# Kernel optimization log

Hardware: AMD Instinct MI355X
Metric: run time of the kernel (lower is better)

The kernel has to match this reference:

```python
import jax, jax.numpy as jnp
import numpy as np


def setup_inputs() -> dict:
    key = jax.random.key(0)
    ks = jax.random.split(key, 5)
    b, t, q_dim, kv_dim, h = 16, 128, 256, 64, 4
    c = t - 1
    q_x = jax.random.normal(ks[0], (b, t, q_dim), dtype=jnp.float32)
    kv_x = jax.random.normal(ks[1], (b, t, c, kv_dim), dtype=jnp.float32)
    # Linear weights stored as [in, out]; no biases (bias=False in torch module).
    sq = 1.0 / np.sqrt(q_dim)
    sk = 1.0 / np.sqrt(kv_dim)
    Wq = jax.random.uniform(ks[2], (q_dim, kv_dim * h), jnp.float32, -sq, sq)
    Wk = jax.random.uniform(ks[3], (kv_dim, kv_dim * h), jnp.float32, -sk, sk)
    Wv = jax.random.uniform(ks[4], (kv_dim, kv_dim * h), jnp.float32, -sk, sk)
    return {"q_x": q_x, "kv_x": kv_x, "Wq": Wq, "Wk": Wk, "Wv": Wv}


def reference(q_x, kv_x, Wq, Wk, Wv):
    b, t, c, k = kv_x.shape  # c = t - 1
    h = Wq.shape[1] // k
    # projections
    q = (q_x @ Wq).reshape(b, t, h, k)          # [b,t,h,k]
    keys = (kv_x @ Wk).reshape(b, t, c, h, k)   # [b,t,c,h,k]
    vals = (kv_x @ Wv).reshape(b, t, c, h, k)
    # per-token attention over the c-sized context
    scores = jnp.einsum('bthk,btchk->bthc', q, keys) / jnp.sqrt(jnp.float32(k))
    w = jax.nn.softmax(scores, axis=-1)          # softmax over context dim
    out = jnp.einsum('bthc,btchk->bthk', w, vals)
    return out.reshape(b, t, h * k)
```

## Files before the change

kernel.cpp:

```cpp
#include <hip/hip_runtime.h>
#include <math.h>

#define Bdim 16
#define Tdim 128
#define Cdim 127
#define Hdim 4
#define QD   256
#define HK   256
#define BT   (Bdim * Tdim)

#define DPP_XOR1        0xB1
#define DPP_XOR2        0x4E
#define DPP_HALF_MIRROR 0x141
#define DPP_MIRROR      0x140
template<int CTRL>
__device__ __forceinline__ float dpp_movf(float x) {
    return __int_as_float(__builtin_amdgcn_update_dpp(
        0, __float_as_int(x), CTRL, 0xF, 0xF, true));
}

__global__ __launch_bounds__(256) void qk_fused(
        const float* __restrict__ q_x,
        const float* __restrict__ Wq,
        const float* __restrict__ Wk,
        float* __restrict__ qk) {
    __shared__ __align__(16) float q_s[4][256];
    __shared__ __align__(16) float p_s[4][4][68];
    int RB = blockIdx.x;
    int tid = threadIdx.x;
    {
        int r = tid >> 6, kq = tid & 63;
        *(float4*)&q_s[r][kq*4] =
            *(const float4*)(q_x + (size_t)(RB*4 + r) * QD + kq * 4);
    }
    __syncthreads();

    float acc[4] = {0.f, 0.f, 0.f, 0.f};
    #pragma unroll 4
    for (int i4 = 0; i4 < 64; ++i4) {
        float w0 = Wq[(size_t)(4*i4+0) * HK + tid];
        float w1 = Wq[(size_t)(4*i4+1) * HK + tid];
        float w2 = Wq[(size_t)(4*i4+2) * HK + tid];
        float w3 = Wq[(size_t)(4*i4+3) * HK + tid];
        #pragma unroll
        for (int r = 0; r < 4; ++r) {
            float4 qv = *(const float4*)&q_s[r][i4*4];
            acc[r] = fmaf(qv.x, w0, fmaf(qv.y, w1, fmaf(qv.z, w2, fmaf(qv.w, w3, acc[r]))));
        }
    }
    int h = tid >> 6, m = tid & 63;
    #pragma unroll
    for (int r = 0; r < 4; ++r) p_s[r][h][m] = acc[r];
    __syncthreads();

    const float4* wk4 = (const float4*)(Wk + (size_t)m * HK + h * 64);
    float4 wkr[16];
    #pragma unroll
    for (int j = 0; j < 16; ++j) wkr[j] = wk4[j];
    float a2[4] = {0.f, 0.f, 0.f, 0.f};
    #pragma unroll
    for (int j4 = 0; j4 < 16; ++j4) {
        #pragma unroll
        for (int r = 0; r < 4; ++r) {
            float4 pv = *(const float4*)&p_s[r][h][j4*4];
            a2[r] = fmaf(pv.x, wkr[j4].x, fmaf(pv.y, wkr[j4].y,
                    fmaf(pv.z, wkr[j4].z, fmaf(pv.w, wkr[j4].w, a2[r]))));
        }
    }
    #pragma unroll
    for (int r = 0; r < 4; ++r)
        qk[(size_t)(RB*4 + r) * HK + tid] = a2[r];
}

__global__ __launch_bounds__(256, 6) void attn_main(
        const float* __restrict__ kv_x,
        const float* __restrict__ qk_g,
        const float* __restrict__ Wv,
        float* __restrict__ out) {
    __shared__ __align__(16) float qk_s[HK];
    __shared__ __align__(16) float4 e4[128];
    __shared__ __align__(16) float4 wx4[Hdim * 16];
    __shared__ __align__(16) float4 reds[4];

    int bt  = blockIdx.x;
    int tid = threadIdx.x;
    const float* Xr = kv_x + (size_t)bt * (Cdim * 64);

    qk_s[tid] = qk_g[(size_t)bt * HK + tid];
    __syncthreads();

    int lane = tid & 63;
    int wave = tid >> 6;

    float e0, e1, e2, e3;
    {
        int c  = tid >> 1;
        int hf = tid & 1;
        bool valid = (c < Cdim);
        int crow = valid ? c : 0;
        const float4* xq = (const float4*)(Xr + crow * 64) + hf * 8;
        const float4* qk4 = (const float4*)qk_s;
        float a0 = 0.f, a1 = 0.f, a2 = 0.f, a3 = 0.f;
        #pragma unroll
        for (int i = 0; i < 8; ++i) {
            float4 xi = xq[i];
            float4 q0 = qk4[0*16 + hf*8 + i];
            float4 q1 = qk4[1*16 + hf*8 + i];
            float4 q2 = qk4[2*16 + hf*8 + i];
            float4 q3 = qk4[3*16 + hf*8 + i];
            a0 = fmaf(q0.x, xi.x, fmaf(q0.y, xi.y, fmaf(q0.z, xi.z, fmaf(q0.w, xi.w, a0))));
            a1 = fmaf(q1.x, xi.x, fmaf(q1.y, xi.y, fmaf(q1.z, xi.z, fmaf(q1.w, xi.w, a1))));
            a2 = fmaf(q2.x, xi.x, fmaf(q2.y, xi.y, fmaf(q2.z, xi.z, fmaf(q2.w, xi.w, a2))));
            a3 = fmaf(q3.x, xi.x, fmaf(q3.y, xi.y, fmaf(q3.z, xi.z, fmaf(q3.w, xi.w, a3))));
        }
        a0 += dpp_movf<DPP_XOR1>(a0);
        a1 += dpp_movf<DPP_XOR1>(a1);
        a2 += dpp_movf<DPP_XOR1>(a2);
        a3 += dpp_movf<DPP_XOR1>(a3);
        e0 = valid ? __expf(a0 * 0.125f) : 0.f;
        e1 = valid ? __expf(a1 * 0.125f) : 0.f;
        e2 = valid ? __expf(a2 * 0.125f) : 0.f;
        e3 = valid ? __expf(a3 * 0.125f) : 0.f;
        if (hf == 0) e4[c] = make_float4(e0, e1, e2, e3);
    }
    float t0 = e0, t1 = e1, t2 = e2, t3 = e3;
    t0 += dpp_movf<DPP_XOR2>(t0); t1 += dpp_movf<DPP_XOR2>(t1);
    t2 += dpp_movf<DPP_XOR2>(t2); t3 += dpp_movf<DPP_XOR2>(t3);
    t0 += dpp_movf<DPP_HALF_MIRROR>(t0); t1 += dpp_movf<DPP_HALF_MIRROR>(t1);
    t2 += dpp_movf<DPP_HALF_MIRROR>(t2); t3 += dpp_movf<DPP_HALF_MIRROR>(t3);
    t0 += dpp_movf<DPP_MIRROR>(t0); t1 += dpp_movf<DPP_MIRROR>(t1);
    t2 += dpp_movf<DPP_MIRROR>(t2); t3 += dpp_movf<DPP_MIRROR>(t3);
    t0 += __shfl_xor(t0, 16, 64); t1 += __shfl_xor(t1, 16, 64);
    t2 += __shfl_xor(t2, 16, 64); t3 += __shfl_xor(t3, 16, 64);
    t0 += __shfl_xor(t0, 32, 64); t1 += __shfl_xor(t1, 32, 64);
    t2 += __shfl_xor(t2, 32, 64); t3 += __shfl_xor(t3, 32, 64);
    if (lane == 0) reds[wave] = make_float4(t0, t1, t2, t3);
    __syncthreads();

    {
        int jc = tid >> 4;
        int g  = tid & 15;
        float4 A0 = {0,0,0,0}, A1 = {0,0,0,0}, A2 = {0,0,0,0}, A3 = {0,0,0,0};
        #pragma unroll
        for (int mm = 0; mm < 8; ++mm) {
            int cc = g + 16 * mm;
            int ccrow = (cc < Cdim) ? cc : 0;
            float4 x4 = *(const float4*)(Xr + ccrow * 64 + jc * 4);
            float4 ee = e4[cc];
            A0.x = fmaf(ee.x, x4.x, A0.x); A0.y = fmaf(ee.x, x4.y, A0.y);
            A0.z = fmaf(ee.x, x4.z, A0.z); A0.w = fmaf(ee.x, x4.w, A0.w);
            A1.x = fmaf(ee.y, x4.x, A1.x); A1.y = fmaf(ee.y, x4.y, A1.y);
            A1.z = fmaf(ee.y, x4.z, A1.z); A1.w = fmaf(ee.y, x4.w, A1.w);
            A2.x = fmaf(ee.z, x4.x, A2.x); A2.y = fmaf(ee.z, x4.y, A2.y);
            A2.z = fmaf(ee.z, x4.z, A2.z); A2.w = fmaf(ee.z, x4.w, A2.w);
            A3.x = fmaf(ee.w, x4.x, A3.x); A3.y = fmaf(ee.w, x4.y, A3.y);
            A3.z = fmaf(ee.w, x4.z, A3.z); A3.w = fmaf(ee.w, x4.w, A3.w);
        }
        #define WXRED(v) \
            v += dpp_movf<DPP_XOR1>(v); \
            v += dpp_movf<DPP_XOR2>(v); \
            v += dpp_movf<DPP_HALF_MIRROR>(v); \
            v += dpp_movf<DPP_MIRROR>(v);
        WXRED(A0.x) WXRED(A0.y) WXRED(A0.z) WXRED(A0.w)
        WXRED(A1.x) WXRED(A1.y) WXRED(A1.z) WXRED(A1.w)
        WXRED(A2.x) WXRED(A2.y) WXRED(A2.z) WXRED(A2.w)
        WXRED(A3.x) WXRED(A3.y) WXRED(A3.z) WXRED(A3.w)
        #undef WXRED
        if ((lane & 15) == 0) {
            wx4[0 * 16 + jc] = A0;
            wx4[1 * 16 + jc] = A1;
            wx4[2 * 16 + jc] = A2;
            wx4[3 * 16 + jc] = A3;
        }
    }
    __syncthreads();

    {
        int hh = tid >> 6, k = tid & 63;
        float4 s0 = reds[0], s1 = reds[1], s2 = reds[2], s3 = reds[3];
        float4 sums = make_float4(s0.x+s1.x+s2.x+s3.x, s0.y+s1.y+s2.y+s3.y,
                                  s0.z+s1.z+s2.z+s3.z, s0.w+s1.w+s2.w+s3.w);
        float denom = (hh == 0) ? sums.x : (hh == 1) ? sums.y
                    : (hh == 2) ? sums.z : sums.w;
        float inv = 1.f / denom;
        const float* wvcol = Wv + hh * 64 + k;
        float acc = 0.f;
        #pragma unroll 4
        for (int jc = 0; jc < 16; ++jc) {
            float4 w4 = wx4[hh * 16 + jc];
            acc = fmaf(w4.x, wvcol[(size_t)(jc*4+0) * HK],
                  fmaf(w4.y, wvcol[(size_t)(jc*4+1) * HK],
                  fmaf(w4.z, wvcol[(size_t)(jc*4+2) * HK],
                  fmaf(w4.w, wvcol[(size_t)(jc*4+3) * HK], acc))));
        }
        out[(size_t)bt * HK + tid] = acc * inv;
    }
}

extern "C" void kernel_launch(void* const* d_in, const int* in_sizes, int n_in,
                              void* d_out, int out_size, void* d_ws, size_t ws_size,
                              hipStream_t stream) {
    const float* q_x  = (const float*)d_in[0];
    const float* kv_x = (const float*)d_in[1];
    const float* Wq   = (const float*)d_in[2];
    const float* Wk   = (const float*)d_in[3];
    const float* Wv   = (const float*)d_in[4];
    float* out = (float*)d_out;

    float* qk = (float*)d_ws;

    qk_fused<<<BT / 4, 256, 0, stream>>>(q_x, Wq, Wk, qk);
    attn_main<<<BT, 256, 0, stream>>>(kv_x, qk, Wv, out);
}
```

Before: 42.55 us.

## Stage kv_x rows in swizzled LDS and prefetch next token while computing

Each attn_main block now handles two (b,t) tokens. It stages the 127x64 kv_x tile into XOR-swizzled shared memory, and loads the second token's tile into registers while the first token is computed, so global latency overlaps compute. Both the score pass and the weighted-sum pass read kv_x from LDS instead of issuing two separate global reads. The cost is about 32KB of LDS, a lower occupancy hint, half as many blocks (1024), and 32 extra registers for the prefetch.

```diff
diff --git a/kernel.cpp b/kernel.cpp
--- a/kernel.cpp
+++ b/kernel.cpp
@@ -72,128 +72,170 @@
         qk[(size_t)(RB*4 + r) * HK + tid] = a2[r];
 }
 
-__global__ __launch_bounds__(256, 6) void attn_main(
+__global__ __launch_bounds__(256, 4) void attn_main(
         const float* __restrict__ kv_x,
         const float* __restrict__ qk_g,
         const float* __restrict__ Wv,
         float* __restrict__ out) {
+    __shared__ __align__(16) float4 sX4[128 * 16];
     __shared__ __align__(16) float qk_s[HK];
     __shared__ __align__(16) float4 e4[128];
     __shared__ __align__(16) float4 wx4[Hdim * 16];
     __shared__ __align__(16) float4 reds[4];
 
-    int bt  = blockIdx.x;
     int tid = threadIdx.x;
-    const float* Xr = kv_x + (size_t)bt * (Cdim * 64);
-
-    qk_s[tid] = qk_g[(size_t)bt * HK + tid];
-    __syncthreads();
-
     int lane = tid & 63;
     int wave = tid >> 6;
-
-    float e0, e1, e2, e3;
+    int bt0 = blockIdx.x * 2;
+
+    int src_off[8];
+    #pragma unroll
+    for (int k = 0; k < 8; ++k) {
+        int l = tid + 256 * k;
+        int c = l >> 4, p = l & 15;
+        src_off[k] = (l < Cdim * 16) ? ((c << 4) + (p ^ (c & 7))) : 0;
+    }
+
+    float4 P[8];
+    float qkp;
     {
+        const float4* Xg = (const float4*)(kv_x + (size_t)bt0 * (Cdim * 64));
+        #pragma unroll
+        for (int k = 0; k < 8; ++k) P[k] = Xg[src_off[k]];
+        qkp = qk_g[(size_t)bt0 * HK + tid];
+    }
+    #pragma unroll
+    for (int k = 0; k < 8; ++k) {
+        int l = tid + 256 * k;
+        sX4[l] = (l < Cdim * 16) ? P[k] : make_float4(0.f, 0.f, 0.f, 0.f);
+    }
+    qk_s[tid] = qkp;
+    __syncthreads();
+
+    #pragma unroll
+    for (int it = 0; it < 2; ++it) {
+        int bt = bt0 + it;
+
+        if (it == 0) {
+            const float4* Xg = (const float4*)(kv_x + (size_t)(bt0+1) * (Cdim * 64));
+            #pragma unroll
+            for (int k = 0; k < 8; ++k) P[k] = Xg[src_off[k]];
+            qkp = qk_g[(size_t)(bt0+1) * HK + tid];
+        }
+
+        float e0, e1, e2, e3;
         int c  = tid >> 1;
-        int hf = tid & 1;
-        bool valid = (c < Cdim);
-        int crow = valid ? c : 0;
-        const float4* xq = (const float4*)(Xr + crow * 64) + hf * 8;
-        const float4* qk4 = (const float4*)qk_s;
-        float a0 = 0.f, a1 = 0.f, a2 = 0.f, a3 = 0.f;
-        #pragma unroll
-        for (int i = 0; i < 8; ++i) {
-            float4 xi = xq[i];
-            float4 q0 = qk4[0*16 + hf*8 + i];
-            float4 q1 = qk4[1*16 + hf*8 + i];
-            float4 q2 = qk4[2*16 + hf*8 + i];
-            float4 q3 = qk4[3*16 + hf*8 + i];
-            a0 = fmaf(q0.x, xi.x, fmaf(q0.y, xi.y, fmaf(q0.z, xi.z, fmaf(q0.w, xi.w, a0))));
-            a1 = fmaf(q1.x, xi.x, fmaf(q1.y, xi.y, fmaf(q1.z, xi.z, fmaf(q1.w, xi.w, a1))));
-            a2 = fmaf(q2.x, xi.x, fmaf(q2.y, xi.y, fmaf(q2.z, xi.z, fmaf(q2.w, xi.w, a2))));
-            a3 = fmaf(q3.x, xi.x, fmaf(q3.y, xi.y, fmaf(q3.z, xi.z, fmaf(q3.w, xi.w, a3))));
-        }
-        a0 += dpp_movf<DPP_XOR1>(a0);
-        a1 += dpp_movf<DPP_XOR1>(a1);
-        a2 += dpp_movf<DPP_XOR1>(a2);
-        a3 += dpp_movf<DPP_XOR1>(a3);
-        e0 = valid ? __expf(a0 * 0.125f) : 0.f;
-        e1 = valid ? __expf(a1 * 0.125f) : 0.f;
-        e2 = valid ? __expf(a2 * 0.125f) : 0.f;
-        e3 = valid ? __expf(a3 * 0.125f) : 0.f;
-        if (hf == 0) e4[c] = make_float4(e0, e1, e2, e3);
-    }
-    float t0 = e0, t1 = e1, t2 = e2, t3 = e3;
-    t0 += dpp_movf<DPP_XOR2>(t0); t1 += dpp_movf<DPP_XOR2>(t1);
-    t2 += dpp_movf<DPP_XOR2>(t2); t3 += dpp_movf<DPP_XOR2>(t3);
-    t0 += dpp_movf<DPP_HALF_MIRROR>(t0); t1 += dpp_movf<DPP_HALF_MIRROR>(t1);
-    t2 += dpp_movf<DPP_HALF_MIRROR>(t2); t3 += dpp_movf<DPP_HALF_MIRROR>(t3);
-    t0 += dpp_movf<DPP_MIRROR>(t0); t1 += dpp_movf<DPP_MIRROR>(t1);
-    t2 += dpp_movf<DPP_MIRROR>(t2); t3 += dpp_movf<DPP_MIRROR>(t3);
-    t0 += __shfl_xor(t0, 16, 64); t1 += __shfl_xor(t1, 16, 64);
-    t2 += __shfl_xor(t2, 16, 64); t3 += __shfl_xor(t3, 16, 64);
-    t0 += __shfl_xor(t0, 32, 64); t1 += __shfl_xor(t1, 32, 64);
-    t2 += __shfl_xor(t2, 32, 64); t3 += __shfl_xor(t3, 32, 64);
-    if (lane == 0) reds[wave] = make_float4(t0, t1, t2, t3);
-    __syncthreads();
-
-    {
-        int jc = tid >> 4;
-        int g  = tid & 15;
-        float4 A0 = {0,0,0,0}, A1 = {0,0,0,0}, A2 = {0,0,0,0}, A3 = {0,0,0,0};
-        #pragma unroll
-        for (int mm = 0; mm < 8; ++mm) {
-            int cc = g + 16 * mm;
-            int ccrow = (cc < Cdim) ? cc : 0;
-            float4 x4 = *(const float4*)(Xr + ccrow * 64 + jc * 4);
-            float4 ee = e4[cc];
-            A0.x = fmaf(ee.x, x4.x, A0.x); A0.y = fmaf(ee.x, x4.y, A0.y);
-            A0.z = fmaf(ee.x, x4.z, A0.z); A0.w = fmaf(ee.x, x4.w, A0.w);
-            A1.x = fmaf(ee.y, x4.x, A1.x); A1.y = fmaf(ee.y, x4.y, A1.y);
-            A1.z = fmaf(ee.y, x4.z, A1.z); A1.w = fmaf(ee.y, x4.w, A1.w);
-            A2.x = fmaf(ee.z, x4.x, A2.x); A2.y = fmaf(ee.z, x4.y, A2.y);
-            A2.z = fmaf(ee.z, x4.z, A2.z); A2.w = fmaf(ee.z, x4.w, A2.w);
-            A3.x = fmaf(ee.w, x4.x, A3.x); A3.y = fmaf(ee.w, x4.y, A3.y);
-            A3.z = fmaf(ee.w, x4.z, A3.z); A3.w = fmaf(ee.w, x4.w, A3.w);
-        }
-        #define WXRED(v) \
-            v += dpp_movf<DPP_XOR1>(v); \
-            v += dpp_movf<DPP_XOR2>(v); \
-            v += dpp_movf<DPP_HALF_MIRROR>(v); \
-            v += dpp_movf<DPP_MIRROR>(v);
-        WXRED(A0.x) WXRED(A0.y) WXRED(A0.z) WXRED(A0.w)
-        WXRED(A1.x) WXRED(A1.y) WXRED(A1.z) WXRED(A1.w)
-        WXRED(A2.x) WXRED(A2.y) WXRED(A2.z) WXRED(A2.w)
-        WXRED(A3.x) WXRED(A3.y) WXRED(A3.z) WXRED(A3.w)
-        #undef WXRED
-        if ((lane & 15) == 0) {
-            wx4[0 * 16 + jc] = A0;
-            wx4[1 * 16 + jc] = A1;
-            wx4[2 * 16 + jc] = A2;
-            wx4[3 * 16 + jc] = A3;
-        }
-    }
-    __syncthreads();
-
-    {
-        int hh = tid >> 6, k = tid & 63;
-        float4 s0 = reds[0], s1 = reds[1], s2 = reds[2], s3 = reds[3];
-        float4 sums = make_float4(s0.x+s1.x+s2.x+s3.x, s0.y+s1.y+s2.y+s3.y,
-                                  s0.z+s1.z+s2.z+s3.z, s0.w+s1.w+s2.w+s3.w);
-        float denom = (hh == 0) ? sums.x : (hh == 1) ? sums.y
-                    : (hh == 2) ? sums.z : sums.w;
-        float inv = 1.f / denom;
-        const float* wvcol = Wv + hh * 64 + k;
-        float acc = 0.f;
-        #pragma unroll 4
-        for (int jc = 0; jc < 16; ++jc) {
-            float4 w4 = wx4[hh * 16 + jc];
-            acc = fmaf(w4.x, wvcol[(size_t)(jc*4+0) * HK],
-                  fmaf(w4.y, wvcol[(size_t)(jc*4+1) * HK],
-                  fmaf(w4.z, wvcol[(size_t)(jc*4+2) * HK],
-                  fmaf(w4.w, wvcol[(size_t)(jc*4+3) * HK], acc))));
-        }
-        out[(size_t)bt * HK + tid] = acc * inv;
+        {
+            int hf = tid & 1;
+            int sw = c & 7;
+            bool valid = (c < Cdim);
+            const float4* xrow = sX4 + c * 16;
+            const float4* qk4 = (const float4*)qk_s;
+            float a0 = 0.f, a1 = 0.f, a2 = 0.f, a3 = 0.f;
+            #pragma unroll
+            for (int i = 0; i < 8; ++i) {
+                float4 xi = xrow[(hf*8 + i) ^ sw];
+                float4 q0 = qk4[0*16 + hf*8 + i];
+                float4 q1 = qk4[1*16 + hf*8 + i];
+                float4 q2 = qk4[2*16 + hf*8 + i];
+                float4 q3 = qk4[3*16 + hf*8 + i];
+                a0 = fmaf(q0.x, xi.x, fmaf(q0.y, xi.y, fmaf(q0.z, xi.z, fmaf(q0.w, xi.w, a0))));
+                a1 = fmaf(q1.x, xi.x, fmaf(q1.y, xi.y, fmaf(q1.z, xi.z, fmaf(q1.w, xi.w, a1))));
+                a2 = fmaf(q2.x, xi.x, fmaf(q2.y, xi.y, fmaf(q2.z, xi.z, fmaf(q2.w, xi.w, a2))));
+                a3 = fmaf(q3.x, xi.x, fmaf(q3.y, xi.y, fmaf(q3.z, xi.z, fmaf(q3.w, xi.w, a3))));
+            }
+            a0 += dpp_movf<DPP_XOR1>(a0);
+            a1 += dpp_movf<DPP_XOR1>(a1);
+            a2 += dpp_movf<DPP_XOR1>(a2);
+            a3 += dpp_movf<DPP_XOR1>(a3);
+            e0 = valid ? __expf(a0 * 0.125f) : 0.f;
+            e1 = valid ? __expf(a1 * 0.125f) : 0.f;
+            e2 = valid ? __expf(a2 * 0.125f) : 0.f;
+            e3 = valid ? __expf(a3 * 0.125f) : 0.f;
+            if (hf == 0) e4[c] = make_float4(e0, e1, e2, e3);
+        }
+        float t0 = e0, t1 = e1, t2 = e2, t3 = e3;
+        t0 += dpp_movf<DPP_XOR2>(t0); t1 += dpp_movf<DPP_XOR2>(t1);
+        t2 += dpp_movf<DPP_XOR2>(t2); t3 += dpp_movf<DPP_XOR2>(t3);
+        t0 += dpp_movf<DPP_HALF_MIRROR>(t0); t1 += dpp_movf<DPP_HALF_MIRROR>(t1);
+        t2 += dpp_movf<DPP_HALF_MIRROR>(t2); t3 += dpp_movf<DPP_HALF_MIRROR>(t3);
+        t0 += dpp_movf<DPP_MIRROR>(t0); t1 += dpp_movf<DPP_MIRROR>(t1);
+        t2 += dpp_movf<DPP_MIRROR>(t2); t3 += dpp_movf<DPP_MIRROR>(t3);
+        t0 += __shfl_xor(t0, 16, 64); t1 += __shfl_xor(t1, 16, 64);
+        t2 += __shfl_xor(t2, 16, 64); t3 += __shfl_xor(t3, 16, 64);
+        t0 += __shfl_xor(t0, 32, 64); t1 += __shfl_xor(t1, 32, 64);
+        t2 += __shfl_xor(t2, 32, 64); t3 += __shfl_xor(t3, 32, 64);
+        if (lane == 0) reds[wave] = make_float4(t0, t1, t2, t3);
+        __syncthreads();
+
+        {
+            int jc = tid >> 4;
+            int g  = tid & 15;
+            int pc = jc ^ (g & 7);
+            float4 A0 = {0,0,0,0}, A1 = {0,0,0,0}, A2 = {0,0,0,0}, A3 = {0,0,0,0};
+            #pragma unroll
+            for (int mm = 0; mm < 8; ++mm) {
+                int cc = g + 16 * mm;
+                float4 x4 = sX4[cc * 16 + pc];
+                float4 ee = e4[cc];
+                A0.x = fmaf(ee.x, x4.x, A0.x); A0.y = fmaf(ee.x, x4.y, A0.y);
+                A0.z = fmaf(ee.x, x4.z, A0.z); A0.w = fmaf(ee.x, x4.w, A0.w);
+                A1.x = fmaf(ee.y, x4.x, A1.x); A1.y = fmaf(ee.y, x4.y, A1.y);
+                A1.z = fmaf(ee.y, x4.z, A1.z); A1.w = fmaf(ee.y, x4.w, A1.w);
+                A2.x = fmaf(ee.z, x4.x, A2.x); A2.y = fmaf(ee.z, x4.y, A2.y);
+                A2.z = fmaf(ee.z, x4.z, A2.z); A2.w = fmaf(ee.z, x4.w, A2.w);
+                A3.x = fmaf(ee.w, x4.x, A3.x); A3.y = fmaf(ee.w, x4.y, A3.y);
+                A3.z = fmaf(ee.w, x4.z, A3.z); A3.w = fmaf(ee.w, x4.w, A3.w);
+            }
+            #define WXRED(v) \
+                v += dpp_movf<DPP_XOR1>(v); \
+                v += dpp_movf<DPP_XOR2>(v); \
+                v += dpp_movf<DPP_HALF_MIRROR>(v); \
+                v += dpp_movf<DPP_MIRROR>(v);
+            WXRED(A0.x) WXRED(A0.y) WXRED(A0.z) WXRED(A0.w)
+            WXRED(A1.x) WXRED(A1.y) WXRED(A1.z) WXRED(A1.w)
+            WXRED(A2.x) WXRED(A2.y) WXRED(A2.z) WXRED(A2.w)
+            WXRED(A3.x) WXRED(A3.y) WXRED(A3.z) WXRED(A3.w)
+            #undef WXRED
+            if ((lane & 15) == 0) {
+                wx4[0 * 16 + jc] = A0;
+                wx4[1 * 16 + jc] = A1;
+                wx4[2 * 16 + jc] = A2;
+                wx4[3 * 16 + jc] = A3;
+            }
+        }
+        __syncthreads();
+
+        if (it == 0) {
+            #pragma unroll
+            for (int k = 0; k < 8; ++k) {
+                int l = tid + 256 * k;
+                sX4[l] = (l < Cdim * 16) ? P[k] : make_float4(0.f, 0.f, 0.f, 0.f);
+            }
+            qk_s[tid] = qkp;
+        }
+
+        {
+            int hh = tid >> 6, k = tid & 63;
+            float4 s0 = reds[0], s1 = reds[1], s2 = reds[2], s3 = reds[3];
+            float4 sums = make_float4(s0.x+s1.x+s2.x+s3.x, s0.y+s1.y+s2.y+s3.y,
+                                      s0.z+s1.z+s2.z+s3.z, s0.w+s1.w+s2.w+s3.w);
+            float denom = (hh == 0) ? sums.x : (hh == 1) ? sums.y
+                        : (hh == 2) ? sums.z : sums.w;
+            float inv = 1.f / denom;
+            const float* wvcol = Wv + hh * 64 + k;
+            float acc = 0.f;
+            #pragma unroll 4
+            for (int jc = 0; jc < 16; ++jc) {
+                float4 w4 = wx4[hh * 16 + jc];
+                acc = fmaf(w4.x, wvcol[(size_t)(jc*4+0) * HK],
+                      fmaf(w4.y, wvcol[(size_t)(jc*4+1) * HK],
+                      fmaf(w4.z, wvcol[(size_t)(jc*4+2) * HK],
+                      fmaf(w4.w, wvcol[(size_t)(jc*4+3) * HK], acc))));
+            }
+            out[(size_t)bt * HK + tid] = acc * inv;
+        }
+        __syncthreads();
     }
 }
 
@@ -210,5 +252,5 @@
     float* qk = (float*)d_ws;
 
     qk_fused<<<BT / 4, 256, 0, stream>>>(q_x, Wq, Wk, qk);
-    attn_main<<<BT, 256, 0, stream>>>(kv_x, qk, Wv, out);
-}
+    attn_main<<<BT / 2, 256, 0, stream>>>(kv_x, qk, Wv, out);
+}
```

Result: faster. 41.42 us (-2.7%).
